# Performance work log

Measured on AMD Instinct MI355X. Metric: run time of the kernel, lower is better.

The kernel has to match this reference:

```python
import jax, jax.numpy as jnp
import numpy as np

# 6 ordered (src, tgt) pairs among 3 modalities, in the same nested-loop order as torch
SRC = jnp.array([0, 0, 1, 1, 2, 2])
TGT = jnp.array([1, 2, 0, 2, 0, 1])

B, L, H, G = 16384, 256, 96, 32
P = 6  # number of translation directions


def _layernorm(x, gamma, beta, eps=1e-5):
    # x: [P, B, F]; gamma/beta: [P, 1, F]
    m = jnp.mean(x, axis=-1, keepdims=True)
    v = jnp.mean((x - m) ** 2, axis=-1, keepdims=True)
    return (x - m) * jax.lax.rsqrt(v + eps) * gamma + beta


def setup_inputs() -> dict:
    key = jax.random.key(0)
    ks = jax.random.split(key, 20)
    f32 = jnp.float32
    d = {}
    d['mus'] = jax.random.normal(ks[0], (3, B, L), f32)
    d['logvars'] = jax.random.normal(ks[1], (3, B, L), f32)
    d['mask'] = jax.random.randint(ks[2], (B, 3), 0, 2).astype(bool)
    # translation head params (stacked over the 6 pairs)
    d['hw1'] = jax.random.normal(ks[3], (P, 2 * L, H), f32) / np.sqrt(2 * L)
    d['hb1'] = jax.random.normal(ks[4], (P, H), f32) * 0.02
    d['hg1'] = jnp.ones((P, H), f32)
    d['hbe1'] = jnp.zeros((P, H), f32)
    d['hw2'] = jax.random.normal(ks[5], (P, H, H), f32) / np.sqrt(H)
    d['hb2'] = jax.random.normal(ks[6], (P, H), f32) * 0.02
    d['hg2'] = jnp.ones((P, H), f32)
    d['hbe2'] = jnp.zeros((P, H), f32)
    d['hw3'] = jax.random.normal(ks[7], (P, H, 2 * L), f32) / np.sqrt(H)
    d['hb3'] = jax.random.normal(ks[8], (P, 2 * L), f32) * 0.02
    # gate network params
    d['gw1'] = jax.random.normal(ks[9], (P, 2 * L, G), f32) / np.sqrt(2 * L)
    d['gb1'] = jax.random.normal(ks[10], (P, G), f32) * 0.02
    d['gg1'] = jnp.ones((P, G), f32)
    d['gbe1'] = jnp.zeros((P, G), f32)
    d['gw2'] = jax.random.normal(ks[11], (P, G, 1), f32) / np.sqrt(G)
    d['gb2'] = jnp.full((P, 1), -1.0, f32)
    return d


def reference(mus, logvars, mask, hw1, hb1, hg1, hbe1, hw2, hb2, hg2, hbe2,
              hw3, hb3, gw1, gb1, gg1, gbe1, gw2, gb2):
    latent = mus.shape[-1]
    # gather source posteriors per pair and concat: [P, B, 2L]
    h = jnp.concatenate([mus[SRC], logvars[SRC]], axis=-1)
    # translation head: Linear -> LN -> GELU (x2) -> Linear
    x = jax.nn.gelu(_layernorm(jnp.einsum('pbi,pih->pbh', h, hw1) + hb1[:, None, :],
                               hg1[:, None, :], hbe1[:, None, :]), approximate=False)
    x = jax.nn.gelu(_layernorm(jnp.einsum('pbh,phk->pbk', x, hw2) + hb2[:, None, :],
                               hg2[:, None, :], hbe2[:, None, :]), approximate=False)
    out = jnp.einsum('pbh,pho->pbo', x, hw3) + hb3[:, None, :]  # [P, B, 2L]
    mu_pseudo = out[..., :latent]
    lv_pseudo = jnp.clip(out[..., latent:], -6.0, 2.0)
    # gate: Linear -> LN -> GELU -> Linear -> sigmoid
    g = jax.nn.gelu(_layernorm(jnp.einsum('pbi,pig->pbg', h, gw1) + gb1[:, None, :],
                               gg1[:, None, :], gbe1[:, None, :]), approximate=False)
    gate = jax.nn.sigmoid(jnp.einsum('pbg,pgo->pbo', g, gw2) + gb2[:, None, :])  # [P, B, 1]
    # only keep rows where source observed and target missing; others are zero-filled
    needs = (mask[:, SRC] & ~mask[:, TGT]).T  # [P, B]
    m3 = needs[:, :, None]
    zero = jnp.zeros((), mu_pseudo.dtype)
    return (jnp.where(m3, mu_pseudo, zero),
            jnp.where(m3, lv_pseudo, zero),
            jnp.where(m3, gate, zero))
```

## Files before the change

### kernel.cpp

```cpp
#include <hip/hip_runtime.h>
#include <hip/hip_bf16.h>
#include <math.h>

#define B_ 16384
#define NP 6

typedef short v8s __attribute__((ext_vector_type(8)));
typedef short v4s __attribute__((ext_vector_type(4)));
typedef float v4f __attribute__((ext_vector_type(4)));

__device__ __forceinline__ float gelu_f(float x) {
    return 0.5f * x * (1.0f + erff(x * 0.7071067811865476f));
}
__device__ __forceinline__ unsigned short f2bf(float f) {
    union { float f; unsigned u; } x; x.f = f;
    unsigned r = x.u + 0x7FFFu + ((x.u >> 16) & 1u);
    return (unsigned short)(r >> 16);
}
__device__ __forceinline__ short bfs(float f) {
    union { __hip_bfloat16 h; unsigned short u; } cv;
    cv.h = __float2bfloat16(f);
    return (short)cv.u;
}
__device__ __forceinline__ void st_nt4(float* p, float a, float b, float c, float d) {
    v4f v = {a, b, c, d};
    __builtin_nontemporal_store(v, (v4f*)p);
}
__device__ __forceinline__ void st_nt1(float* p, float v) {
    __builtin_nontemporal_store(v, p);
}

__global__ __launch_bounds__(256) void k_prep(
    const float* __restrict__ hw1, const float* __restrict__ gw1,
    const float* __restrict__ hw2, const float* __restrict__ hw3,
    unsigned short* __restrict__ w1t, unsigned short* __restrict__ w2f,
    unsigned short* __restrict__ w3f)
{
    const int T1 = NP * 65536, T2 = NP * 9216, T3 = NP * 49152;
    for (int i = blockIdx.x * 256 + threadIdx.x; i < T1 + T2 + T3; i += gridDim.x * 256) {
        if (i < T1) {
            int p = i >> 16, rem = i & 65535, c = rem >> 9, k = rem & 511;
            float v = (c < 96) ? hw1[p * 49152 + k * 96 + c] : gw1[p * 16384 + k * 32 + (c - 96)];
            w1t[i] = f2bf(v);
        } else if (i < T1 + T2) {
            int j2 = i - T1, p = j2 / 9216, rem = j2 % 9216;
            int f = rem >> 9, within = rem & 511;
            int qg = within >> 3, j = within & 7;
            int q = qg >> 2, g = qg & 3;
            int k = (f % 3) * 32 + g * 8 + j;
            int col = (f / 3) * 16 + q;
            w2f[j2] = f2bf(hw2[p * 9216 + k * 96 + col]);
        } else {
            int j3 = i - T1 - T2, p = j3 / 49152, rem = j3 % 49152;
            int f = rem >> 9, within = rem & 511;
            int qg = within >> 3, j = within & 7;
            int q = qg >> 2, g = qg & 3;
            int k = (f % 3) * 32 + g * 8 + j;
            int col = (f / 3) * 16 + q;
            w3f[j3] = f2bf(hw3[p * 49152 + k * 512 + col]);
        }
    }
}

__global__ __launch_bounds__(256) void k_count(
    const int* __restrict__ mask, int* __restrict__ counts,
    int* __restrict__ lists, unsigned long long* __restrict__ nb)
{
    int p   = blockIdx.x >> 3;
    int seg = blockIdx.x & 7;
    int src = p >> 1;
    int tgt = (0x102021 >> (p * 4)) & 0xF;
    int t = threadIdx.x;
    int lane = t & 63;
    for (int it = 0; it < 8; ++it) {
        int b = seg * 2048 + it * 256 + t;
        int needs = (mask[b * 3 + src] != 0) && (mask[b * 3 + tgt] == 0);
        unsigned long long bal = __ballot(needs);
        int total = __popcll(bal);
        int base = 0;
        if (lane == 0) {
            nb[p * 256 + (b >> 6)] = bal;
            if (total) base = atomicAdd(&counts[p], total);
        }
        base = __shfl(base, 0, 64);
        if (needs) {
            int prefix = __popcll(bal & ((1ull << lane) - 1ull));
            lists[p * B_ + base + prefix] = b;
        }
    }
}

__global__ __launch_bounds__(512, 2) void k_main(
    const float* __restrict__ mus, const float* __restrict__ logvars,
    const unsigned short* __restrict__ w1t, const unsigned short* __restrict__ w2f,
    const unsigned short* __restrict__ w3f,
    const float* __restrict__ hb1, const float* __restrict__ hg1, const float* __restrict__ hbe1,
    const float* __restrict__ hb2, const float* __restrict__ hg2, const float* __restrict__ hbe2,
    const float* __restrict__ hb3,
    const float* __restrict__ gb1, const float* __restrict__ gg1, const float* __restrict__ gbe1,
    const float* __restrict__ gw2, const float* __restrict__ gb2,
    const int* __restrict__ counts, const int* __restrict__ lists,
    const unsigned long long* __restrict__ nb,
    float* __restrict__ out0, float* __restrict__ out1, float* __restrict__ out2)
{
    int cb = blockIdx.x;
    int p  = cb % 6, blk = cb / 6;
    int t  = threadIdx.x;
    int w  = t >> 6, l = t & 63, g = l >> 4, q = l & 15;
    int cnt = counts[p];

    __shared__ __align__(16) unsigned short smW[128 * 512];
    __shared__ __align__(16) unsigned short smX[8 * 1664];

    const unsigned short* w1p = w1t + (size_t)p * 65536;
    const unsigned short* w2p = w2f + (size_t)p * 9216;
    const unsigned short* w3p = w3f + (size_t)p * 49152;

    {
        int c = t >> 2, qt = t & 3;
        const unsigned short* src = w1p + c * 512 + qt * 128;
        unsigned short* dstrow = smW + c * 512;
        int cx = c & 7;
#pragma unroll
        for (int jj = 0; jj < 16; ++jj) {
            int j = qt * 16 + jj;
            *(v8s*)(dstrow + (((j ^ cx)) << 3)) = *(const v8s*)(src + jj * 8);
        }
    }
    __syncthreads();

    unsigned short* mX = smX + w * 1664;
    float gb2p = gb2[p];

    int start = (blk * 8 + w) * 16;
    if (start < cnt) {
        int nr = min(16, cnt - start);
        int myrow = lists[p * B_ + min(start + q, cnt - 1)];
        const float* Ab = mus     + (size_t)(p >> 1) * B_ * 256 + (size_t)myrow * 256 + g * 8;
        const float* Lb = logvars + (size_t)(p >> 1) * B_ * 256 + (size_t)myrow * 256 + g * 8;

        v4f acc1[8];
#pragma unroll
        for (int n = 0; n < 8; ++n) acc1[n] = (v4f){0.f, 0.f, 0.f, 0.f};

        int qx = q & 7;
#pragma unroll 4
        for (int kt = 0; kt < 16; ++kt) {
            const float* ap = ((kt < 8) ? Ab : Lb) + (kt & 7) * 32;
            float4 f0 = *(const float4*)ap;
            float4 f1 = *(const float4*)(ap + 4);
            v8s a;
            a[0] = bfs(f0.x); a[1] = bfs(f0.y); a[2] = bfs(f0.z); a[3] = bfs(f0.w);
            a[4] = bfs(f1.x); a[5] = bfs(f1.y); a[6] = bfs(f1.z); a[7] = bfs(f1.w);
#pragma unroll
            for (int n = 0; n < 8; ++n) {
                int col = n * 16 + q;
                int i = kt * 4 + g;
                v8s b = *(const v8s*)(smW + col * 512 + ((i ^ qx) << 3));
                acc1[n] = __builtin_amdgcn_mfma_f32_16x16x32_bf16(b, a, acc1[n], 0, 0, 0);
            }
        }

        {
            float vb[8][4];
#pragma unroll
            for (int n = 0; n < 8; ++n) {
                float4 bb = (n < 6) ? *(const float4*)(hb1 + p * 96 + n * 16 + 4 * g)
                                    : *(const float4*)(gb1 + p * 32 + (n - 6) * 16 + 4 * g);
                vb[n][0] = acc1[n][0] + bb.x; vb[n][1] = acc1[n][1] + bb.y;
                vb[n][2] = acc1[n][2] + bb.z; vb[n][3] = acc1[n][3] + bb.w;
            }
            float hs = 0.f;
#pragma unroll
            for (int n = 0; n < 6; ++n)
#pragma unroll
                for (int j = 0; j < 4; ++j) hs += vb[n][j];
            hs += __shfl_xor(hs, 16, 64); hs += __shfl_xor(hs, 32, 64);
            float mean = hs * (1.f / 96.f);
            float sq = 0.f;
#pragma unroll
            for (int n = 0; n < 6; ++n)
#pragma unroll
                for (int j = 0; j < 4; ++j) { float d = vb[n][j] - mean; sq += d * d; }
            sq += __shfl_xor(sq, 16, 64); sq += __shfl_xor(sq, 32, 64);
            float rs = rsqrtf(sq * (1.f / 96.f) + 1e-5f);
#pragma unroll
            for (int n = 0; n < 6; ++n) {
                float4 ga = *(const float4*)(hg1  + p * 96 + n * 16 + 4 * g);
                float4 be = *(const float4*)(hbe1 + p * 96 + n * 16 + 4 * g);
                v4s xo;
                xo[0] = bfs(gelu_f((vb[n][0] - mean) * rs * ga.x + be.x));
                xo[1] = bfs(gelu_f((vb[n][1] - mean) * rs * ga.y + be.y));
                xo[2] = bfs(gelu_f((vb[n][2] - mean) * rs * ga.z + be.z));
                xo[3] = bfs(gelu_f((vb[n][3] - mean) * rs * ga.w + be.w));
                *(v4s*)(mX + q * 104 + n * 16 + 4 * g) = xo;
            }
            float gs = 0.f;
#pragma unroll
            for (int n = 6; n < 8; ++n)
#pragma unroll
                for (int j = 0; j < 4; ++j) gs += vb[n][j];
            gs += __shfl_xor(gs, 16, 64); gs += __shfl_xor(gs, 32, 64);
            float mg = gs * (1.f / 32.f);
            float gq = 0.f;
#pragma unroll
            for (int n = 6; n < 8; ++n)
#pragma unroll
                for (int j = 0; j < 4; ++j) { float d = vb[n][j] - mg; gq += d * d; }
            gq += __shfl_xor(gq, 16, 64); gq += __shfl_xor(gq, 32, 64);
            float rg = rsqrtf(gq * (1.f / 32.f) + 1e-5f);
            float gv = 0.f;
#pragma unroll
            for (int n = 6; n < 8; ++n) {
                int cg = (n - 6) * 16 + 4 * g;
                float4 ga = *(const float4*)(gg1  + p * 32 + cg);
                float4 be = *(const float4*)(gbe1 + p * 32 + cg);
                float4 w2 = *(const float4*)(gw2  + p * 32 + cg);
                gv += gelu_f((vb[n][0] - mg) * rg * ga.x + be.x) * w2.x;
                gv += gelu_f((vb[n][1] - mg) * rg * ga.y + be.y) * w2.y;
                gv += gelu_f((vb[n][2] - mg) * rg * ga.z + be.z) * w2.z;
                gv += gelu_f((vb[n][3] - mg) * rg * ga.w + be.w) * w2.w;
            }
            gv += __shfl_xor(gv, 16, 64); gv += __shfl_xor(gv, 32, 64);
            if (g == 0 && q < nr)
                st_nt1(out2 + p * B_ + myrow, 1.f / (1.f + expf(-(gv + gb2p))));
        }

        {
            v4f acc2[6];
#pragma unroll
            for (int n = 0; n < 6; ++n) acc2[n] = (v4f){0.f, 0.f, 0.f, 0.f};
            int fo = q * 32 + g * 8;
#pragma unroll
            for (int kit = 0; kit < 3; ++kit) {
                v8s xa = *(const v8s*)(mX + q * 104 + kit * 32 + g * 8);
#pragma unroll
                for (int n = 0; n < 6; ++n) {
                    v8s wb = *(const v8s*)(w2p + (n * 3 + kit) * 512 + fo);
                    acc2[n] = __builtin_amdgcn_mfma_f32_16x16x32_bf16(wb, xa, acc2[n], 0, 0, 0);
                }
            }
            float vc[6][4];
#pragma unroll
            for (int n = 0; n < 6; ++n) {
                float4 bb = *(const float4*)(hb2 + p * 96 + n * 16 + 4 * g);
                vc[n][0] = acc2[n][0] + bb.x; vc[n][1] = acc2[n][1] + bb.y;
                vc[n][2] = acc2[n][2] + bb.z; vc[n][3] = acc2[n][3] + bb.w;
            }
            float hs = 0.f;
#pragma unroll
            for (int n = 0; n < 6; ++n)
#pragma unroll
                for (int j = 0; j < 4; ++j) hs += vc[n][j];
            hs += __shfl_xor(hs, 16, 64); hs += __shfl_xor(hs, 32, 64);
            float mean = hs * (1.f / 96.f);
            float sq = 0.f;
#pragma unroll
            for (int n = 0; n < 6; ++n)
#pragma unroll
                for (int j = 0; j < 4; ++j) { float d = vc[n][j] - mean; sq += d * d; }
            sq += __shfl_xor(sq, 16, 64); sq += __shfl_xor(sq, 32, 64);
            float rs = rsqrtf(sq * (1.f / 96.f) + 1e-5f);
#pragma unroll
            for (int n = 0; n < 6; ++n) {
                float4 ga = *(const float4*)(hg2  + p * 96 + n * 16 + 4 * g);
                float4 be = *(const float4*)(hbe2 + p * 96 + n * 16 + 4 * g);
                v4s xo;
                xo[0] = bfs(gelu_f((vc[n][0] - mean) * rs * ga.x + be.x));
                xo[1] = bfs(gelu_f((vc[n][1] - mean) * rs * ga.y + be.y));
                xo[2] = bfs(gelu_f((vc[n][2] - mean) * rs * ga.z + be.z));
                xo[3] = bfs(gelu_f((vc[n][3] - mean) * rs * ga.w + be.w));
                *(v4s*)(mX + q * 104 + n * 16 + 4 * g) = xo;
            }
        }

        {
            size_t base = ((size_t)(p * B_ + myrow)) * 256;
            int fo = q * 32 + g * 8;
#pragma unroll 1
            for (int pc = 0; pc < 4; ++pc) {
                v4f acc3[8];
#pragma unroll
                for (int n = 0; n < 8; ++n) acc3[n] = (v4f){0.f, 0.f, 0.f, 0.f};
#pragma unroll
                for (int kit = 0; kit < 3; ++kit) {
                    v8s xa = *(const v8s*)(mX + q * 104 + kit * 32 + g * 8);
#pragma unroll
                    for (int n = 0; n < 8; ++n) {
                        v8s wb = *(const v8s*)(w3p + ((pc * 8 + n) * 3 + kit) * 512 + fo);
                        acc3[n] = __builtin_amdgcn_mfma_f32_16x16x32_bf16(wb, xa, acc3[n], 0, 0, 0);
                    }
                }
#pragma unroll
                for (int n = 0; n < 8; ++n) {
                    int c = pc * 128 + n * 16 + 4 * g;
                    float4 bb = *(const float4*)(hb3 + p * 512 + c);
                    if (q < nr) {
                        float o0 = acc3[n][0] + bb.x, o1 = acc3[n][1] + bb.y;
                        float o2 = acc3[n][2] + bb.z, o3 = acc3[n][3] + bb.w;
                        if (pc < 2) {
                            st_nt4(out0 + base + c, o0, o1, o2, o3);
                        } else {
                            o0 = fminf(fmaxf(o0, -6.f), 2.f); o1 = fminf(fmaxf(o1, -6.f), 2.f);
                            o2 = fminf(fmaxf(o2, -6.f), 2.f); o3 = fminf(fmaxf(o3, -6.f), 2.f);
                            st_nt4(out1 + base + c - 256, o0, o1, o2, o3);
                        }
                    }
                }
            }
        }
    }

    {
        int zbase = cb * 384 + w * 48;
        for (int i = 0; i < 48; ++i) {
            int grow = zbase + i;
            int zp = grow >> 14, zr = grow & 16383;
            if (!((nb[zp * 256 + (zr >> 6)] >> (zr & 63)) & 1ull)) {
                size_t rb = ((size_t)zp * B_ + zr) * 256 + l * 4;
                st_nt4(out0 + rb, 0.f, 0.f, 0.f, 0.f);
                st_nt4(out1 + rb, 0.f, 0.f, 0.f, 0.f);
                if (l == 0) st_nt1(out2 + zp * B_ + zr, 0.f);
            }
        }
    }
}

extern "C" void kernel_launch(void* const* d_in, const int* in_sizes, int n_in,
                              void* d_out, int out_size, void* d_ws, size_t ws_size,
                              hipStream_t stream)
{
    (void)in_sizes; (void)n_in; (void)out_size; (void)ws_size;

    const float* mus     = (const float*)d_in[0];
    const float* logvars = (const float*)d_in[1];
    const int*   mask    = (const int*)d_in[2];
    const float* hw1  = (const float*)d_in[3];
    const float* hb1  = (const float*)d_in[4];
    const float* hg1  = (const float*)d_in[5];
    const float* hbe1 = (const float*)d_in[6];
    const float* hw2  = (const float*)d_in[7];
    const float* hb2  = (const float*)d_in[8];
    const float* hg2  = (const float*)d_in[9];
    const float* hbe2 = (const float*)d_in[10];
    const float* hw3  = (const float*)d_in[11];
    const float* hb3  = (const float*)d_in[12];
    const float* gw1  = (const float*)d_in[13];
    const float* gb1  = (const float*)d_in[14];
    const float* gg1  = (const float*)d_in[15];
    const float* gbe1 = (const float*)d_in[16];
    const float* gw2  = (const float*)d_in[17];
    const float* gb2  = (const float*)d_in[18];

    float* out0 = (float*)d_out;
    float* out1 = out0 + (size_t)NP * B_ * 256;
    float* out2 = out1 + (size_t)NP * B_ * 256;

    int* counts = (int*)d_ws;
    int* lists  = counts + 16;
    unsigned short* w1t = (unsigned short*)(lists + NP * B_);
    unsigned short* w2f = w1t + (size_t)NP * 65536;
    unsigned short* w3f = w2f + (size_t)NP * 9216;
    unsigned long long* nbm = (unsigned long long*)(w3f + (size_t)NP * 49152);

    hipMemsetAsync(d_ws, 0, 64, stream);
    k_count<<<dim3(NP * 8), dim3(256), 0, stream>>>(mask, counts, lists, nbm);
    k_prep<<<dim3(512), dim3(256), 0, stream>>>(hw1, gw1, hw2, hw3, w1t, w2f, w3f);
    k_main<<<dim3(256), dim3(512), 0, stream>>>(
        mus, logvars, w1t, w2f, w3f,
        hb1, hg1, hbe1, hb2, hg2, hbe2, hb3,
        gb1, gg1, gbe1, gw2, gb2,
        counts, lists, nbm, out0, out1, out2);
}
```

Measured before the change: 110.5 us.

## Zero outputs with memset, prefetch source rows before weight staging, drop nontemporal stores

Replaces the in-kernel masked zero-fill, which used a per-row needs bitmask, with a full-output hipMemsetAsync, then lets k_main overwrite only the active rows. The mus rows are loaded into registers before the shared-memory weight staging and barrier, and logvars loads are issued while the mus half of the first GEMM runs, to hide global latency. Nontemporal stores become ordinary stores. The cost is that the memset writes the whole ~100MB output, including rows that are later overwritten, and the prefetch raises register pressure.

```diff
diff --git a/kernel.cpp b/kernel.cpp
--- a/kernel.cpp
+++ b/kernel.cpp
@@ -21,13 +21,6 @@
     union { __hip_bfloat16 h; unsigned short u; } cv;
     cv.h = __float2bfloat16(f);
     return (short)cv.u;
-}
-__device__ __forceinline__ void st_nt4(float* p, float a, float b, float c, float d) {
-    v4f v = {a, b, c, d};
-    __builtin_nontemporal_store(v, (v4f*)p);
-}
-__device__ __forceinline__ void st_nt1(float* p, float v) {
-    __builtin_nontemporal_store(v, p);
 }
 
 __global__ __launch_bounds__(256) void k_prep(
@@ -63,8 +56,7 @@
 }
 
 __global__ __launch_bounds__(256) void k_count(
-    const int* __restrict__ mask, int* __restrict__ counts,
-    int* __restrict__ lists, unsigned long long* __restrict__ nb)
+    const int* __restrict__ mask, int* __restrict__ counts, int* __restrict__ lists)
 {
     int p   = blockIdx.x >> 3;
     int seg = blockIdx.x & 7;
@@ -78,10 +70,7 @@
         unsigned long long bal = __ballot(needs);
         int total = __popcll(bal);
         int base = 0;
-        if (lane == 0) {
-            nb[p * 256 + (b >> 6)] = bal;
-            if (total) base = atomicAdd(&counts[p], total);
-        }
+        if (lane == 0 && total) base = atomicAdd(&counts[p], total);
         base = __shfl(base, 0, 64);
         if (needs) {
             int prefix = __popcll(bal & ((1ull << lane) - 1ull));
@@ -100,7 +89,6 @@
     const float* __restrict__ gb1, const float* __restrict__ gg1, const float* __restrict__ gbe1,
     const float* __restrict__ gw2, const float* __restrict__ gb2,
     const int* __restrict__ counts, const int* __restrict__ lists,
-    const unsigned long long* __restrict__ nb,
     float* __restrict__ out0, float* __restrict__ out1, float* __restrict__ out2)
 {
     int cb = blockIdx.x;
@@ -116,6 +104,22 @@
     const unsigned short* w2p = w2f + (size_t)p * 9216;
     const unsigned short* w3p = w3f + (size_t)p * 49152;
 
+    int start = (blk * 8 + w) * 16;
+    bool active = start < cnt;
+    int nr = active ? min(16, cnt - start) : 0;
+    int myrow = active ? lists[p * B_ + min(start + q, cnt - 1)] : 0;
+    const float* Ab = mus     + (size_t)(p >> 1) * B_ * 256 + (size_t)myrow * 256 + g * 8;
+    const float* Lb = logvars + (size_t)(p >> 1) * B_ * 256 + (size_t)myrow * 256 + g * 8;
+
+    float4 ma[8], mb[8];
+    if (active) {
+#pragma unroll
+        for (int k = 0; k < 8; ++k) {
+            ma[k] = *(const float4*)(Ab + k * 32);
+            mb[k] = *(const float4*)(Ab + k * 32 + 4);
+        }
+    }
+
     {
         int c = t >> 2, qt = t & 3;
         const unsigned short* src = w1p + c * 512 + qt * 128;
@@ -132,31 +136,36 @@
     unsigned short* mX = smX + w * 1664;
     float gb2p = gb2[p];
 
-    int start = (blk * 8 + w) * 16;
-    if (start < cnt) {
-        int nr = min(16, cnt - start);
-        int myrow = lists[p * B_ + min(start + q, cnt - 1)];
-        const float* Ab = mus     + (size_t)(p >> 1) * B_ * 256 + (size_t)myrow * 256 + g * 8;
-        const float* Lb = logvars + (size_t)(p >> 1) * B_ * 256 + (size_t)myrow * 256 + g * 8;
-
+    if (active) {
         v4f acc1[8];
 #pragma unroll
         for (int n = 0; n < 8; ++n) acc1[n] = (v4f){0.f, 0.f, 0.f, 0.f};
 
         int qx = q & 7;
-#pragma unroll 4
-        for (int kt = 0; kt < 16; ++kt) {
-            const float* ap = ((kt < 8) ? Ab : Lb) + (kt & 7) * 32;
-            float4 f0 = *(const float4*)ap;
-            float4 f1 = *(const float4*)(ap + 4);
+        float4 la[8], lb[8];
+#pragma unroll
+        for (int kt = 0; kt < 8; ++kt) {
+            la[kt] = *(const float4*)(Lb + kt * 32);
+            lb[kt] = *(const float4*)(Lb + kt * 32 + 4);
             v8s a;
-            a[0] = bfs(f0.x); a[1] = bfs(f0.y); a[2] = bfs(f0.z); a[3] = bfs(f0.w);
-            a[4] = bfs(f1.x); a[5] = bfs(f1.y); a[6] = bfs(f1.z); a[7] = bfs(f1.w);
+            a[0] = bfs(ma[kt].x); a[1] = bfs(ma[kt].y); a[2] = bfs(ma[kt].z); a[3] = bfs(ma[kt].w);
+            a[4] = bfs(mb[kt].x); a[5] = bfs(mb[kt].y); a[6] = bfs(mb[kt].z); a[7] = bfs(mb[kt].w);
 #pragma unroll
             for (int n = 0; n < 8; ++n) {
-                int col = n * 16 + q;
                 int i = kt * 4 + g;
-                v8s b = *(const v8s*)(smW + col * 512 + ((i ^ qx) << 3));
+                v8s b = *(const v8s*)(smW + (n * 16 + q) * 512 + ((i ^ qx) << 3));
+                acc1[n] = __builtin_amdgcn_mfma_f32_16x16x32_bf16(b, a, acc1[n], 0, 0, 0);
+            }
+        }
+#pragma unroll
+        for (int kt = 0; kt < 8; ++kt) {
+            v8s a;
+            a[0] = bfs(la[kt].x); a[1] = bfs(la[kt].y); a[2] = bfs(la[kt].z); a[3] = bfs(la[kt].w);
+            a[4] = bfs(lb[kt].x); a[5] = bfs(lb[kt].y); a[6] = bfs(lb[kt].z); a[7] = bfs(lb[kt].w);
+#pragma unroll
+            for (int n = 0; n < 8; ++n) {
+                int i = (kt + 8) * 4 + g;
+                v8s b = *(const v8s*)(smW + (n * 16 + q) * 512 + ((i ^ qx) << 3));
                 acc1[n] = __builtin_amdgcn_mfma_f32_16x16x32_bf16(b, a, acc1[n], 0, 0, 0);
             }
         }
@@ -223,7 +232,7 @@
             }
             gv += __shfl_xor(gv, 16, 64); gv += __shfl_xor(gv, 32, 64);
             if (g == 0 && q < nr)
-                st_nt1(out2 + p * B_ + myrow, 1.f / (1.f + expf(-(gv + gb2p))));
+                out2[p * B_ + myrow] = 1.f / (1.f + expf(-(gv + gb2p)));
         }
 
         {
@@ -299,28 +308,14 @@
                         float o0 = acc3[n][0] + bb.x, o1 = acc3[n][1] + bb.y;
                         float o2 = acc3[n][2] + bb.z, o3 = acc3[n][3] + bb.w;
                         if (pc < 2) {
-                            st_nt4(out0 + base + c, o0, o1, o2, o3);
+                            *(float4*)(out0 + base + c) = make_float4(o0, o1, o2, o3);
                         } else {
                             o0 = fminf(fmaxf(o0, -6.f), 2.f); o1 = fminf(fmaxf(o1, -6.f), 2.f);
                             o2 = fminf(fmaxf(o2, -6.f), 2.f); o3 = fminf(fmaxf(o3, -6.f), 2.f);
-                            st_nt4(out1 + base + c - 256, o0, o1, o2, o3);
+                            *(float4*)(out1 + base + c - 256) = make_float4(o0, o1, o2, o3);
                         }
                     }
                 }
-            }
-        }
-    }
-
-    {
-        int zbase = cb * 384 + w * 48;
-        for (int i = 0; i < 48; ++i) {
-            int grow = zbase + i;
-            int zp = grow >> 14, zr = grow & 16383;
-            if (!((nb[zp * 256 + (zr >> 6)] >> (zr & 63)) & 1ull)) {
-                size_t rb = ((size_t)zp * B_ + zr) * 256 + l * 4;
-                st_nt4(out0 + rb, 0.f, 0.f, 0.f, 0.f);
-                st_nt4(out1 + rb, 0.f, 0.f, 0.f, 0.f);
-                if (l == 0) st_nt1(out2 + zp * B_ + zr, 0.f);
             }
         }
     }
@@ -330,7 +325,7 @@
                               void* d_out, int out_size, void* d_ws, size_t ws_size,
                               hipStream_t stream)
 {
-    (void)in_sizes; (void)n_in; (void)out_size; (void)ws_size;
+    (void)in_sizes; (void)n_in; (void)ws_size;
 
     const float* mus     = (const float*)d_in[0];
     const float* logvars = (const float*)d_in[1];
@@ -361,14 +356,14 @@
     unsigned short* w1t = (unsigned short*)(lists + NP * B_);
     unsigned short* w2f = w1t + (size_t)NP * 65536;
     unsigned short* w3f = w2f + (size_t)NP * 9216;
-    unsigned long long* nbm = (unsigned long long*)(w3f + (size_t)NP * 49152);
-
+
+    hipMemsetAsync(d_out, 0, (size_t)out_size * sizeof(float), stream);
     hipMemsetAsync(d_ws, 0, 64, stream);
-    k_count<<<dim3(NP * 8), dim3(256), 0, stream>>>(mask, counts, lists, nbm);
+    k_count<<<dim3(NP * 8), dim3(256), 0, stream>>>(mask, counts, lists);
     k_prep<<<dim3(512), dim3(256), 0, stream>>>(hw1, gw1, hw2, hw3, w1t, w2f, w3f);
     k_main<<<dim3(256), dim3(512), 0, stream>>>(
         mus, logvars, w1t, w2f, w3f,
         hb1, hg1, hbe1, hb2, hg2, hbe2, hb3,
         gb1, gg1, gbe1, gw2, gb2,
-        counts, lists, nbm, out0, out1, out2);
-}
+        counts, lists, out0, out1, out2);
+}
```

New measurement: 105.3 us. 1.05x faster.
